# Kernel optimization log

Hardware: AMD Instinct MI355X
Metric: run time of the kernel (lower is better)

## Reference

```python
import jax, jax.numpy as jnp
import numpy as np

B, TQ, TK, F, H = 8, 2048, 2048, 1024, 1024


def setup_inputs() -> dict:
    key = jax.random.key(0)
    ks = jax.random.split(key, 9)
    scale = 1.0 / np.sqrt(F)
    query = jax.random.normal(ks[0], (B, TQ, F), dtype=jnp.float32)
    encoder_states = jax.random.normal(ks[1], (B, TK, F), dtype=jnp.float32)
    # boolean attention mask; True = keep. Random Bernoulli(0.5).
    target_mask = jax.random.randint(ks[2], (B, TQ, TK), 0, 2) > 0
    # Linear params (torch nn.Linear: y = x @ W.T + b); store W as [F, H] for x @ W.
    Wq = jax.random.normal(ks[3], (F, H), dtype=jnp.float32) * scale
    bq = jax.random.normal(ks[4], (H,), dtype=jnp.float32) * scale
    Wk = jax.random.normal(ks[5], (F, H), dtype=jnp.float32) * scale
    bk = jax.random.normal(ks[6], (H,), dtype=jnp.float32) * scale
    Wv = jax.random.normal(ks[7], (F, H), dtype=jnp.float32) * scale
    bv = jax.random.normal(ks[8], (H,), dtype=jnp.float32) * scale
    return {"query": query, "encoder_states": encoder_states, "target_mask": target_mask,
            "Wq": Wq, "bq": bq, "Wk": Wk, "bk": bk, "Wv": Wv, "bv": bv}


def reference(query, encoder_states, target_mask, Wq, bq, Wk, bk, Wv, bv):
    # init(): K/V projections of encoder states
    K = jnp.einsum('btf,fh->bth', encoder_states, Wk) + bk   # [B,TK,H]
    V = jnp.einsum('btf,fh->bth', encoder_states, Wv) + bv   # [B,TK,H]
    # forward()
    Q = jnp.einsum('btf,fh->bth', query, Wq) + bq            # [B,TQ,H]
    scores = jnp.einsum('bqh,bkh->bqk', Q, K) / jnp.sqrt(jnp.asarray(H, Q.dtype))
    scores = jnp.where(target_mask, scores, -jnp.inf)
    attn = jax.nn.softmax(scores, axis=-1)                   # [B,TQ,TK]
    return jnp.einsum('bqk,bkh->bqh', attn, V)               # [B,TQ,H]
```

## Files before the change

### kernel.cpp

```cpp
#include <hip/hip_runtime.h>

#define NB 8
#define TQv 2048
#define TKv 2048
#define FD 1024
#define HD 1024

typedef __attribute__((ext_vector_type(8))) short short8;
typedef __attribute__((ext_vector_type(8))) _Float16 half8;
typedef __attribute__((ext_vector_type(16))) float f32x16;

__device__ __forceinline__ short f2bf(float f) {
    union { float f; unsigned u; } v; v.f = f;
    unsigned r = v.u + 0x7FFFu + ((v.u >> 16) & 1u);
    return (short)(r >> 16);
}

__device__ __forceinline__ void async16(const short* g, short* l) {
    __builtin_amdgcn_global_load_lds(
        (const __attribute__((address_space(1))) unsigned int*)g,
        (__attribute__((address_space(3))) unsigned int*)l, 16, 0, 0);
}

template <bool F16>
__device__ __forceinline__ void gemm128_core(const short* __restrict__ A, int lda,
                                             const short* __restrict__ B, int ldb,
                                             int K, short* As, short* Bs,
                                             f32x16 acc[2][2], int tid) {
    int wave = tid >> 6, lane = tid & 63;
    int lrow = lane >> 2;
    int lcol = (lane & 3) << 3;
    const short* ga0 = A + (size_t)(wave * 32 + lrow) * lda + lcol;
    const short* ga1 = ga0 + (size_t)16 * lda;
    const short* gb0 = B + (size_t)(wave * 32 + lrow) * ldb + lcol;
    const short* gb1 = gb0 + (size_t)16 * ldb;
    short* la0 = As + (wave * 32) * 32;
    short* la1 = As + (wave * 32 + 16) * 32;
    short* lb0 = Bs + (wave * 32) * 32;
    short* lb1 = Bs + (wave * 32 + 16) * 32;
    int mbase = (wave & 1) * 64 + (lane & 31);
    int nbase = (wave >> 1) * 64 + (lane & 31);
    int kh = (lane >> 5) << 3;

    for (int k0 = 0; k0 < K; k0 += 32) {
        __syncthreads();
        async16(ga0, la0);
        async16(ga1, la1);
        async16(gb0, lb0);
        async16(gb1, lb1);
        ga0 += 32; ga1 += 32; gb0 += 32; gb1 += 32;
        __syncthreads();
        if (F16) {
            half8 af[2][2], bf[2][2];
#pragma unroll
            for (int mt = 0; mt < 2; ++mt)
#pragma unroll
                for (int ks = 0; ks < 2; ++ks) {
                    af[mt][ks] = *(const half8*)(As + (mbase + mt * 32) * 32 + ks * 16 + kh);
                    bf[mt][ks] = *(const half8*)(Bs + (nbase + mt * 32) * 32 + ks * 16 + kh);
                }
#pragma unroll
            for (int ks = 0; ks < 2; ++ks)
#pragma unroll
                for (int mt = 0; mt < 2; ++mt)
#pragma unroll
                    for (int nt = 0; nt < 2; ++nt)
                        acc[mt][nt] = __builtin_amdgcn_mfma_f32_32x32x16_f16(
                            af[mt][ks], bf[nt][ks], acc[mt][nt], 0, 0, 0);
        } else {
            short8 af[2][2], bf[2][2];
#pragma unroll
            for (int mt = 0; mt < 2; ++mt)
#pragma unroll
                for (int ks = 0; ks < 2; ++ks) {
                    af[mt][ks] = *(const short8*)(As + (mbase + mt * 32) * 32 + ks * 16 + kh);
                    bf[mt][ks] = *(const short8*)(Bs + (nbase + mt * 32) * 32 + ks * 16 + kh);
                }
#pragma unroll
            for (int ks = 0; ks < 2; ++ks)
#pragma unroll
                for (int mt = 0; mt < 2; ++mt)
#pragma unroll
                    for (int nt = 0; nt < 2; ++nt)
                        acc[mt][nt] = __builtin_amdgcn_mfma_f32_32x32x16_bf16(
                            af[mt][ks], bf[nt][ks], acc[mt][nt], 0, 0, 0);
        }
    }
}
#define ACC0 {0.f,0.f,0.f,0.f,0.f,0.f,0.f,0.f,0.f,0.f,0.f,0.f,0.f,0.f,0.f,0.f}
#define ACC_INIT {{ACC0, ACC0}, {ACC0, ACC0}}
#define EPI_GM(mt, r) (tile_m + (wave & 1) * 64 + (mt) * 32 + ((lane >> 5) << 2) + (((r) >> 2) << 3) + ((r) & 3))
#define EPI_GN(nt)    (tile_n + (wave >> 1) * 64 + (nt) * 32 + (lane & 31))

__global__ __launch_bounds__(256) void convert_kernel(const float* __restrict__ q,
                                                      const float* __restrict__ e,
                                                      short* __restrict__ xq,
                                                      short* __restrict__ xe) {
    size_t i = (size_t)blockIdx.x * 256 + threadIdx.x;
    const float* src = blockIdx.y ? e : q;
    short* dst = blockIdx.y ? xe : xq;
    float4 a = ((const float4*)src)[2 * i];
    float4 b = ((const float4*)src)[2 * i + 1];
    short8 v;
    v[0] = f2bf(a.x); v[1] = f2bf(a.y); v[2] = f2bf(a.z); v[3] = f2bf(a.w);
    v[4] = f2bf(b.x); v[5] = f2bf(b.y); v[6] = f2bf(b.z); v[7] = f2bf(b.w);
    ((short8*)dst)[i] = v;
}

__global__ __launch_bounds__(256) void wtrans_kernel(const float* __restrict__ Wq,
                                                     const float* __restrict__ Wk,
                                                     const float* __restrict__ Wv,
                                                     short* __restrict__ Wt) {
    __shared__ float tile[32][33];
    const float* W = (blockIdx.z == 0) ? Wq : (blockIdx.z == 1) ? Wk : Wv;
    short* dst = Wt + (size_t)blockIdx.z * HD * FD;
    int h0 = blockIdx.x * 32, f0 = blockIdx.y * 32;
    int tx = threadIdx.x, ty = threadIdx.y;
    for (int j = ty; j < 32; j += 8)
        tile[j][tx] = W[(size_t)(f0 + j) * HD + h0 + tx];
    __syncthreads();
    for (int j = ty; j < 32; j += 8)
        dst[(size_t)(h0 + j) * FD + f0 + tx] = f2bf(tile[tx][j]);
}

__global__ __launch_bounds__(256, 4) void projqk_kernel(const short* __restrict__ Xq,
                                                        const short* __restrict__ Xe,
                                                        const short* __restrict__ Wt3,
                                                        const float* __restrict__ bq,
                                                        const float* __restrict__ bk,
                                                        short* __restrict__ Q,
                                                        short* __restrict__ K) {
    __shared__ short As[128 * 32];
    __shared__ short Bs[128 * 32];
    int tid = threadIdx.x;
    int wave = tid >> 6, lane = tid & 63;
    int p = blockIdx.z;
    const short* X = (p == 0) ? Xq : Xe;
    const short* Wt = Wt3 + (size_t)p * HD * FD;
    const float* bias = (p == 0) ? bq : bk;
    short* O = (p == 0) ? Q : K;
    int bid = blockIdx.x;
    int xcd = bid & 7;
    int idx = bid >> 3;
    int n_t = idx & 7;
    int m_t = (idx >> 3) * 8 + xcd;
    int tile_m = m_t * 128;
    int tile_n = n_t * 128;
    f32x16 acc[2][2] = ACC_INIT;
    gemm128_core<false>(X + (size_t)tile_m * FD, FD, Wt + (size_t)tile_n * FD, FD, FD,
                        As, Bs, acc, tid);
#pragma unroll
    for (int nt = 0; nt < 2; ++nt) {
        int gn = EPI_GN(nt);
        float bv_ = bias[gn];
#pragma unroll
        for (int mt = 0; mt < 2; ++mt)
#pragma unroll
            for (int r = 0; r < 16; ++r) {
                int gm = EPI_GM(mt, r);
                O[(size_t)gm * HD + gn] = f2bf(acc[mt][nt][r] + bv_);
            }
    }
}

__global__ __launch_bounds__(256, 4) void projv_kernel(const short* __restrict__ Xe,
                                                       const short* __restrict__ Wtv,
                                                       const float* __restrict__ bv,
                                                       short* __restrict__ Vt) {
    __shared__ short As[128 * 32];
    __shared__ short Bs[128 * 32];
    int tid = threadIdx.x;
    int wave = tid >> 6, lane = tid & 63;
    int id = blockIdx.x;
    int b = id & 7;
    int i = id >> 3;
    int n_t = i & 15;
    int m_t = i >> 4;
    int tile_m = m_t * 128;
    int tile_n = n_t * 128;
    const short* Xb = Xe + (size_t)b * TKv * FD;
    f32x16 acc[2][2] = ACC_INIT;
    gemm128_core<false>(Wtv + (size_t)tile_m * FD, FD, Xb + (size_t)tile_n * FD, FD, FD,
                        As, Bs, acc, tid);
    short* Ob = Vt + (size_t)b * HD * TKv;
#pragma unroll
    for (int mt = 0; mt < 2; ++mt)
#pragma unroll
        for (int r = 0; r < 16; ++r) {
            int gm = EPI_GM(mt, r);
            float bv_ = bv[gm];
#pragma unroll
            for (int nt = 0; nt < 2; ++nt) {
                int gn = EPI_GN(nt);
                union { _Float16 h; short s; } cv;
                cv.h = (_Float16)(acc[mt][nt][r] + bv_);
                Ob[(size_t)gm * TKv + gn] = cv.s;
            }
        }
}

__global__ __launch_bounds__(256) void maskbits_kernel(const int* __restrict__ mask,
                                                       unsigned long long* __restrict__ Mbits,
                                                       float* __restrict__ L) {
    int tid = threadIdx.x;
    int lane = tid & 63;
    if (blockIdx.x < 64) L[blockIdx.x * 256 + tid] = 0.f;
    const int NW = NB * TQv * (TKv / 64);
    int stride = gridDim.x * 4;
    for (int w = blockIdx.x * 4 + (tid >> 6); w < NW; w += stride) {
        int v = mask[(size_t)w * 64 + lane];
        unsigned long long bal = __ballot(v != 0);
        if (lane == 0) Mbits[w] = bal;
    }
}

__global__ __launch_bounds__(256, 4) void score_kernel(const short* __restrict__ Q,
                                                       const short* __restrict__ K,
                                                       const unsigned long long* __restrict__ Mbits,
                                                       short* __restrict__ S,
                                                       float* __restrict__ L) {
    __shared__ short As[128 * 32];
    __shared__ short Bs[128 * 32];
    int tid = threadIdx.x;
    int wave = tid >> 6, lane = tid & 63;
    int id = blockIdx.x;
    int b = id & 7;
    int i = id >> 3;
    int n_t = i & 15;
    int m_t = i >> 4;
    int tile_m = m_t * 128;
    int tile_n = n_t * 128;
    const short* Aq = Q + (size_t)b * TQv * HD;
    const short* Bk = K + (size_t)b * TKv * HD;
    f32x16 acc[2][2] = ACC_INIT;
    gemm128_core<false>(Aq + (size_t)tile_m * HD, HD, Bk + (size_t)tile_n * HD, HD, HD,
                        As, Bs, acc, tid);
    short* Sb = S + (size_t)b * TQv * TKv;
    const unsigned long long* Mb = Mbits + (size_t)b * TQv * (TKv / 64);
    float* Lb = L + (size_t)b * TQv;
    int wofs = (tile_n >> 6) + (wave >> 1);
    int l31 = lane & 31;
#pragma unroll
    for (int mt = 0; mt < 2; ++mt)
#pragma unroll
        for (int r = 0; r < 16; ++r) {
            int gm = EPI_GM(mt, r);
            unsigned long long bits = Mb[(size_t)gm * (TKv / 64) + wofs];
            float rs = 0.f;
#pragma unroll
            for (int nt = 0; nt < 2; ++nt) {
                int gn = EPI_GN(nt);
                float s = acc[mt][nt][r] * 0.03125f;
                float p = ((bits >> (nt * 32 + l31)) & 1ULL)
                              ? exp2f((s - 4.0f) * 1.44269504f) : 0.f;
                rs += p;
                union { _Float16 h; short sh; } cv;
                cv.h = (_Float16)p;
                Sb[(size_t)gm * TKv + gn] = cv.sh;
            }
            for (int sh = 1; sh < 32; sh <<= 1) rs += __shfl_xor(rs, sh);
            if (l31 == 0) atomicAdd(&Lb[gm], rs);
        }
}

__global__ __launch_bounds__(256, 4) void pv_kernel(const short* __restrict__ P,
                                                    const short* __restrict__ Vt,
                                                    const float* __restrict__ L,
                                                    float* __restrict__ Out) {
    __shared__ short As[128 * 32];
    __shared__ short Bs[128 * 32];
    int tid = threadIdx.x;
    int wave = tid >> 6, lane = tid & 63;
    int id = blockIdx.x;
    int b = id & 7;
    int i = id >> 3;
    int n_t = i & 7;
    int m_t = i >> 3;
    int tile_m = m_t * 128;
    int tile_n = n_t * 128;
    const short* Ap = P + (size_t)b * TQv * TKv;
    const short* Bv = Vt + (size_t)b * HD * TKv;
    const float* Lb = L + (size_t)b * TQv;
    f32x16 acc[2][2] = ACC_INIT;
    gemm128_core<true>(Ap + (size_t)tile_m * TKv, TKv, Bv + (size_t)tile_n * TKv, TKv, TKv,
                       As, Bs, acc, tid);
    float* Ob = Out + (size_t)b * TQv * HD;
#pragma unroll
    for (int mt = 0; mt < 2; ++mt)
#pragma unroll
        for (int r = 0; r < 16; ++r) {
            int gm = EPI_GM(mt, r);
            float l = Lb[gm];
            float inv = (l > 0.f) ? 1.f / l : 0.f;
#pragma unroll
            for (int nt = 0; nt < 2; ++nt) {
                int gn = EPI_GN(nt);
                Ob[(size_t)gm * HD + gn] = acc[mt][nt][r] * inv;
            }
        }
}

extern "C" void kernel_launch(void* const* d_in, const int* in_sizes, int n_in,
                              void* d_out, int out_size, void* d_ws, size_t ws_size,
                              hipStream_t stream) {
    const float* query = (const float*)d_in[0];
    const float* enc   = (const float*)d_in[1];
    const int*   mask  = (const int*)d_in[2];
    const float* Wq    = (const float*)d_in[3];
    const float* bq    = (const float*)d_in[4];
    const float* Wk    = (const float*)d_in[5];
    const float* bk    = (const float*)d_in[6];
    const float* Wv    = (const float*)d_in[7];
    const float* bv    = (const float*)d_in[8];
    float* out = (float*)d_out;

    char* ws = (char*)d_ws;
    short* Wt  = (short*)(ws);
    unsigned long long* Mbits = (unsigned long long*)(ws);
    float* L   = (float*)(ws + 4194304);
    short* Xq  = (short*)(ws + 6291456);
    short* Xe  = (short*)(ws + 39845888);
    short* S   = (short*)(ws + 6291456);
    short* Qb  = (short*)(ws + 73400320);
    short* Kb  = (short*)(ws + 106954752);
    short* Vt  = (short*)(ws + 140509184);
    (void)in_sizes; (void)n_in; (void)out_size; (void)ws_size;

    convert_kernel<<<dim3(8192, 2), 256, 0, stream>>>(query, enc, Xq, Xe);
    wtrans_kernel<<<dim3(32, 32, 3), dim3(32, 8), 0, stream>>>(Wq, Wk, Wv, Wt);
    projqk_kernel<<<dim3(1024, 1, 2), 256, 0, stream>>>(Xq, Xe, Wt, bq, bk, Qb, Kb);
    projv_kernel<<<dim3(1024), 256, 0, stream>>>(Xe, Wt + (size_t)2 * HD * FD, bv, Vt);
    maskbits_kernel<<<dim3(2048), 256, 0, stream>>>(mask, Mbits, L);
    score_kernel<<<dim3(2048), 256, 0, stream>>>(Qb, Kb, Mbits, S, L);
    pv_kernel<<<dim3(1024), 256, 0, stream>>>(S, Vt, L, out);
}
```

Before: 667.4 us.

## Double K-step to 64 and XOR-swizzle LDS tiles in shared GEMM core

The shared 128x128 GEMM core now stages 64-wide K slices instead of 32, which halves the number of barrier pairs per GEMM, and it doubles the LDS tile buffers in all four kernels to match. The global-to-LDS async loads and the fragment reads use an XOR swizzle on the 16-byte chunk index to avoid LDS bank conflicts. The cost is twice the LDS per block, which may lower occupancy. There is still no double-buffering, so loads and MFMA work are not overlapped.

```diff
diff --git a/kernel.cpp b/kernel.cpp
--- a/kernel.cpp
+++ b/kernel.cpp
@@ -28,62 +28,61 @@
                                              int K, short* As, short* Bs,
                                              f32x16 acc[2][2], int tid) {
     int wave = tid >> 6, lane = tid & 63;
-    int lrow = lane >> 2;
-    int lcol = (lane & 3) << 3;
-    const short* ga0 = A + (size_t)(wave * 32 + lrow) * lda + lcol;
-    const short* ga1 = ga0 + (size_t)16 * lda;
-    const short* gb0 = B + (size_t)(wave * 32 + lrow) * ldb + lcol;
-    const short* gb1 = gb0 + (size_t)16 * ldb;
-    short* la0 = As + (wave * 32) * 32;
-    short* la1 = As + (wave * 32 + 16) * 32;
-    short* lb0 = Bs + (wave * 32) * 32;
-    short* lb1 = Bs + (wave * 32 + 16) * 32;
+    int lr = lane >> 3;
+    int kc = (lane & 7) ^ lr;
+    const short* ga[4]; const short* gb[4];
+    short* la[4]; short* lb[4];
+#pragma unroll
+    for (int j = 0; j < 4; ++j) {
+        int w = wave + 4 * j;
+        ga[j] = A + (size_t)(8 * w + lr) * lda + kc * 8;
+        gb[j] = B + (size_t)(8 * w + lr) * ldb + kc * 8;
+        la[j] = As + w * 512;
+        lb[j] = Bs + w * 512;
+    }
     int mbase = (wave & 1) * 64 + (lane & 31);
     int nbase = (wave >> 1) * 64 + (lane & 31);
-    int kh = (lane >> 5) << 3;
-
-    for (int k0 = 0; k0 < K; k0 += 32) {
+    int khalf = lane >> 5;
+    int l7 = lane & 7;
+
+    for (int k0 = 0; k0 < K; k0 += 64) {
         __syncthreads();
-        async16(ga0, la0);
-        async16(ga1, la1);
-        async16(gb0, lb0);
-        async16(gb1, lb1);
-        ga0 += 32; ga1 += 32; gb0 += 32; gb1 += 32;
+#pragma unroll
+        for (int j = 0; j < 4; ++j) { async16(ga[j], la[j]); async16(gb[j], lb[j]); }
+#pragma unroll
+        for (int j = 0; j < 4; ++j) { ga[j] += 64; gb[j] += 64; }
         __syncthreads();
-        if (F16) {
-            half8 af[2][2], bf[2][2];
-#pragma unroll
-            for (int mt = 0; mt < 2; ++mt)
-#pragma unroll
-                for (int ks = 0; ks < 2; ++ks) {
-                    af[mt][ks] = *(const half8*)(As + (mbase + mt * 32) * 32 + ks * 16 + kh);
-                    bf[mt][ks] = *(const half8*)(Bs + (nbase + mt * 32) * 32 + ks * 16 + kh);
+#pragma unroll
+        for (int ks = 0; ks < 4; ++ks) {
+            int kcc = 2 * ks + khalf;
+            int sw = kcc ^ l7;
+            if (F16) {
+                half8 af[2], bf[2];
+#pragma unroll
+                for (int mt = 0; mt < 2; ++mt) {
+                    af[mt] = *(const half8*)(As + ((mbase + mt * 32) * 8 + sw) * 8);
+                    bf[mt] = *(const half8*)(Bs + ((nbase + mt * 32) * 8 + sw) * 8);
                 }
-#pragma unroll
-            for (int ks = 0; ks < 2; ++ks)
 #pragma unroll
                 for (int mt = 0; mt < 2; ++mt)
 #pragma unroll
                     for (int nt = 0; nt < 2; ++nt)
                         acc[mt][nt] = __builtin_amdgcn_mfma_f32_32x32x16_f16(
-                            af[mt][ks], bf[nt][ks], acc[mt][nt], 0, 0, 0);
-        } else {
-            short8 af[2][2], bf[2][2];
-#pragma unroll
-            for (int mt = 0; mt < 2; ++mt)
-#pragma unroll
-                for (int ks = 0; ks < 2; ++ks) {
-                    af[mt][ks] = *(const short8*)(As + (mbase + mt * 32) * 32 + ks * 16 + kh);
-                    bf[mt][ks] = *(const short8*)(Bs + (nbase + mt * 32) * 32 + ks * 16 + kh);
+                            af[mt], bf[nt], acc[mt][nt], 0, 0, 0);
+            } else {
+                short8 af[2], bf[2];
+#pragma unroll
+                for (int mt = 0; mt < 2; ++mt) {
+                    af[mt] = *(const short8*)(As + ((mbase + mt * 32) * 8 + sw) * 8);
+                    bf[mt] = *(const short8*)(Bs + ((nbase + mt * 32) * 8 + sw) * 8);
                 }
-#pragma unroll
-            for (int ks = 0; ks < 2; ++ks)
 #pragma unroll
                 for (int mt = 0; mt < 2; ++mt)
 #pragma unroll
                     for (int nt = 0; nt < 2; ++nt)
                         acc[mt][nt] = __builtin_amdgcn_mfma_f32_32x32x16_bf16(
-                            af[mt][ks], bf[nt][ks], acc[mt][nt], 0, 0, 0);
+                            af[mt], bf[nt], acc[mt][nt], 0, 0, 0);
+            }
         }
     }
 }
@@ -130,8 +129,8 @@
                                                         const float* __restrict__ bk,
                                                         short* __restrict__ Q,
                                                         short* __restrict__ K) {
-    __shared__ short As[128 * 32];
-    __shared__ short Bs[128 * 32];
+    __shared__ short As[128 * 64];
+    __shared__ short Bs[128 * 64];
     int tid = threadIdx.x;
     int wave = tid >> 6, lane = tid & 63;
     int p = blockIdx.z;
@@ -167,8 +166,8 @@
                                                        const short* __restrict__ Wtv,
                                                        const float* __restrict__ bv,
                                                        short* __restrict__ Vt) {
-    __shared__ short As[128 * 32];
-    __shared__ short Bs[128 * 32];
+    __shared__ short As[128 * 64];
+    __shared__ short Bs[128 * 64];
     int tid = threadIdx.x;
     int wave = tid >> 6, lane = tid & 63;
     int id = blockIdx.x;
@@ -219,8 +218,8 @@
                                                        const unsigned long long* __restrict__ Mbits,
                                                        short* __restrict__ S,
                                                        float* __restrict__ L) {
-    __shared__ short As[128 * 32];
-    __shared__ short Bs[128 * 32];
+    __shared__ short As[128 * 64];
+    __shared__ short Bs[128 * 64];
     int tid = threadIdx.x;
     int wave = tid >> 6, lane = tid & 63;
     int id = blockIdx.x;
@@ -267,8 +266,8 @@
                                                     const short* __restrict__ Vt,
                                                     const float* __restrict__ L,
                                                     float* __restrict__ Out) {
-    __shared__ short As[128 * 32];
-    __shared__ short Bs[128 * 32];
+    __shared__ short As[128 * 64];
+    __shared__ short Bs[128 * 64];
     int tid = threadIdx.x;
     int wave = tid >> 6, lane = tid & 63;
     int id = blockIdx.x;
```

Result: faster. 629.0 us (-5.7%).
